# Optimization experiments

Measured on AMD Instinct MI355X. Metric: run time of the kernel, lower is better.

## Reference

```python
import jax, jax.numpy as jnp
import numpy as np

H_D, W_D = 64, 64          # 1024x1024 image / 16 patch size
N = H_D * W_D              # 4096 patches
D = 768                    # DINO ViT-B/16 embed dim
ALPHA = 0.5
K = 100


def setup_inputs() -> dict:
    key = jax.random.key(0)
    k1, k2 = jax.random.split(key)
    out = jax.random.normal(k1, (N, D), dtype=jnp.float32)
    attn_seed = jax.random.randint(k2, (2,), 0, H_D, dtype=jnp.int32)
    return {"out": out, "attn_seed": attn_seed}


def _connected_components(mask):
    """8-connectivity connected components via iterative min-label propagation.
    Background = 0. Foreground pixels get the minimum initial id (+1) of their
    component (same partition as cv2.connectedComponents, different numbering)."""
    fg = mask > 0
    BIG = jnp.int32(N + 1)
    init = jnp.where(fg, jnp.arange(N, dtype=jnp.int32).reshape(H_D, W_D) + 1, BIG)

    def step(l):
        p = jnp.pad(l, 1, constant_values=N + 1)
        m = l
        for dy in (0, 1, 2):          # fixed 3x3 neighborhood, not a data-dim loop
            for dx in (0, 1, 2):
                m = jnp.minimum(m, p[dy:dy + H_D, dx:dx + W_D])
        return jnp.where(fg, m, BIG)

    def cond(st):
        l, prev = st
        return jnp.any(l != prev)

    def body(st):
        l, _ = st
        return step(l), l

    l, _ = jax.lax.while_loop(cond, body, (step(init), init))
    return jnp.where(fg, l, 0)


def reference(out, attn_seed):
    # similarity between all patch features: [N, N]
    sim = out @ out.T
    deg = sim >= 0                                        # degree_matrix (bool)
    # patch with fewest non-negative similarities
    seed_degree_flat = jnp.argmin(deg.sum(axis=0)).astype(jnp.int32)
    seed_degree = jnp.stack([seed_degree_flat // W_D, seed_degree_flat % W_D])
    # blend degree seed with attention seed
    seed_rc = jnp.round(ALPHA * seed_degree + (1.0 - ALPHA) * attn_seed).astype(jnp.int32)
    seed = seed_rc[0] * W_D + seed_rc[1]

    # initial expansion set = patches positively correlated with the seed
    s = deg[seed].astype(jnp.int32)
    s = s.at[seed].set(1)                                 # degree_matrix[seed][seed] = 255 (truthy)
    order = jnp.argsort(-sim[seed])                       # descending
    s = s.at[order[K:]].set(0)                            # keep top-k most similar

    # sequential seed expansion (updates feed into later iterations)
    def step(s, i):
        grows = jnp.sum(sim[i] * (s == 1)) > 0
        s = s.at[i].set(jnp.where(s[i] == 0, 0, jnp.where(grows, 1, 0)))
        return s, None

    s, _ = jax.lax.scan(step, s, jnp.arange(N))

    return _connected_components(s.reshape(H_D, W_D))
```

## Files before the change

kernel.cpp:

```cpp
#include <hip/hip_runtime.h>
#include <cstdint>

#define NP   4096
#define DD   768
#define HD   64
#define WD   64
#define KTOP 100
#define BIGL 4097

typedef short bf16x8 __attribute__((ext_vector_type(8)));
typedef float f32x4  __attribute__((ext_vector_type(4)));

__device__ __forceinline__ void gload_lds16(const void* g, void* l) {
    __builtin_amdgcn_global_load_lds(
        (const __attribute__((address_space(1))) unsigned int*)(uintptr_t)g,
        (__attribute__((address_space(3))) unsigned int*)(unsigned int)(uintptr_t)l,
        16, 0, 0);
}

__device__ __forceinline__ unsigned short f2bf_rne(float x) {
    unsigned b = __float_as_uint(x);
    unsigned r = b + 0x7FFFu + ((b >> 16) & 1u);
    return (unsigned short)(r >> 16);
}
__device__ __forceinline__ float bf2f(unsigned short h) {
    return __uint_as_float(((unsigned)h) << 16);
}

__global__ __launch_bounds__(256) void k_split(const float* __restrict__ A,
                                               unsigned short* __restrict__ hi,
                                               unsigned short* __restrict__ lo,
                                               int* __restrict__ counts) {
    if (blockIdx.x < 16) counts[blockIdx.x * 256 + threadIdx.x] = 0;
    int idx = blockIdx.x * 256 + threadIdx.x;
    float4 v = ((const float4*)A)[idx];
    unsigned short h0 = f2bf_rne(v.x), h1 = f2bf_rne(v.y),
                   h2 = f2bf_rne(v.z), h3 = f2bf_rne(v.w);
    unsigned short l0 = f2bf_rne(v.x - bf2f(h0)), l1 = f2bf_rne(v.y - bf2f(h1)),
                   l2 = f2bf_rne(v.z - bf2f(h2)), l3 = f2bf_rne(v.w - bf2f(h3));
    ((ushort4*)hi)[idx] = make_ushort4(h0, h1, h2, h3);
    ((ushort4*)lo)[idx] = make_ushort4(l0, l1, l2, l3);
}

__device__ __forceinline__ void stage_group(const unsigned short* __restrict__ hi,
                                            const unsigned short* __restrict__ lo,
                                            int i0, int j0, int kbase, int tid,
                                            unsigned short* G) {
#pragma unroll
    for (int q = 0; q < 8; ++q) {
        int pp = q * 256 + tid;
        int ppt = pp & 1023;
        int row = ppt >> 3;
        int kcl = (ppt & 7) ^ (row & 7);
        int rbase = (pp < 1024) ? i0 : j0;
        const unsigned short* src =
            ((kcl < 4) ? hi : lo) + (size_t)(rbase + row) * DD + kbase + (kcl & 3) * 8;
        gload_lds16(src, G + pp * 8);
    }
}

__global__ __launch_bounds__(256, 2) void k_gemm(const unsigned short* __restrict__ hi,
                                                 const unsigned short* __restrict__ lo,
                                                 int* __restrict__ counts) {
    __shared__ __align__(16) unsigned short G[2][2048 * 8];

    int t = ((blockIdx.x & 7) * 66) + (blockIdx.x >> 3);
    int SI = 0, SJ = 0, rem = t;
    for (;;) {
        int sz = (SI == SJ) ? 36 : 64;
        if (rem < sz) break;
        rem -= sz;
        if (++SJ == 4) { ++SI; SJ = SI; }
    }
    int li, lj;
    if (SI == SJ) {
        int r = 0;
        while (rem >= (8 - r)) { rem -= (8 - r); ++r; }
        li = r; lj = r + rem;
    } else { li = rem >> 3; lj = rem & 7; }
    int bi = SI * 8 + li, bj = SJ * 8 + lj;
    int i0 = bi * 128, j0 = bj * 128;

    int tid = threadIdx.x;
    int lane = tid & 63, w = tid >> 6;
    int wm = w & 1, wn = w >> 1;

    f32x4 acc[4][4];
#pragma unroll
    for (int ti = 0; ti < 4; ++ti)
#pragma unroll
        for (int u = 0; u < 4; ++u) { acc[ti][u][0] = 0.f; acc[ti][u][1] = 0.f;
                                      acc[ti][u][2] = 0.f; acc[ti][u][3] = 0.f; }

    int kcf = lane >> 4;
    int paH[4], paL[4], pbH[4], pbL[4];
#pragma unroll
    for (int tt = 0; tt < 4; ++tt) {
        int arow = wm * 64 + tt * 16 + (lane & 15);
        paH[tt] = arow * 8 + (kcf ^ (arow & 7));
        paL[tt] = arow * 8 + ((kcf + 4) ^ (arow & 7));
    }
#pragma unroll
    for (int u = 0; u < 4; ++u) {
        int brow = wn * 64 + u * 16 + (lane & 15);
        pbH[u] = 1024 + brow * 8 + (kcf ^ (brow & 7));
        pbL[u] = 1024 + brow * 8 + ((kcf + 4) ^ (brow & 7));
    }

    stage_group(hi, lo, i0, j0, 0, tid, G[0]);
    for (int it = 0; it < 24; ++it) {
        int cur = it & 1;
        asm volatile("s_waitcnt vmcnt(0)" ::: "memory");
        __builtin_amdgcn_s_barrier();

        bf16x8 ahi[4], alo[4], bhi[4], blo[4];
#pragma unroll
        for (int tt = 0; tt < 4; ++tt) {
            ahi[tt] = *(const bf16x8*)&G[cur][paH[tt] * 8];
            alo[tt] = *(const bf16x8*)&G[cur][paL[tt] * 8];
        }
#pragma unroll
        for (int u = 0; u < 4; ++u) {
            bhi[u] = *(const bf16x8*)&G[cur][pbH[u] * 8];
            blo[u] = *(const bf16x8*)&G[cur][pbL[u] * 8];
        }

        if (it + 1 < 24)
            stage_group(hi, lo, i0, j0, (it + 1) * 32, tid, G[cur ^ 1]);

        __builtin_amdgcn_s_setprio(1);
#pragma unroll
        for (int ti = 0; ti < 4; ++ti)
#pragma unroll
            for (int u = 0; u < 4; ++u) {
                acc[ti][u] = __builtin_amdgcn_mfma_f32_16x16x32_bf16(
                    ahi[ti], bhi[u], acc[ti][u], 0, 0, 0);
                acc[ti][u] = __builtin_amdgcn_mfma_f32_16x16x32_bf16(
                    alo[ti], bhi[u], acc[ti][u], 0, 0, 0);
                acc[ti][u] = __builtin_amdgcn_mfma_f32_16x16x32_bf16(
                    ahi[ti], blo[u], acc[ti][u], 0, 0, 0);
            }
        __builtin_amdgcn_s_setprio(0);
    }

    __syncthreads();
    int* colc = (int*)&G[0][0];
    int* rowc = ((int*)&G[0][0]) + 128;
    if (tid < 128) { colc[tid] = 0; rowc[tid] = 0; }
    __syncthreads();

    int nl = lane & 15;
    int rg = lane >> 4;
#pragma unroll
    for (int u = 0; u < 4; ++u) {
        int v = 0;
#pragma unroll
        for (int ti = 0; ti < 4; ++ti) {
            f32x4 a = acc[ti][u];
            v += ((a[0] >= 0.f) ? 1 : 0) + ((a[1] >= 0.f) ? 1 : 0) +
                 ((a[2] >= 0.f) ? 1 : 0) + ((a[3] >= 0.f) ? 1 : 0);
        }
        v += __shfl_xor(v, 16);
        v += __shfl_xor(v, 32);
        if (rg == 0) atomicAdd(&colc[wn * 64 + u * 16 + nl], v);
    }
    if (bi != bj) {
#pragma unroll
        for (int ti = 0; ti < 4; ++ti)
#pragma unroll
            for (int g = 0; g < 4; ++g) {
                int rv = ((acc[ti][0][g] >= 0.f) ? 1 : 0) +
                         ((acc[ti][1][g] >= 0.f) ? 1 : 0) +
                         ((acc[ti][2][g] >= 0.f) ? 1 : 0) +
                         ((acc[ti][3][g] >= 0.f) ? 1 : 0);
                rv += __shfl_xor(rv, 1);
                rv += __shfl_xor(rv, 2);
                rv += __shfl_xor(rv, 4);
                rv += __shfl_xor(rv, 8);
                if (nl == 0) atomicAdd(&rowc[wm * 64 + ti * 16 + rg * 4 + g], rv);
            }
    }
    __syncthreads();
    if (tid < 128) {
        atomicAdd(&counts[j0 + tid], colc[tid]);
        if (bi != bj) atomicAdd(&counts[i0 + tid], rowc[tid]);
    }
}

__device__ __forceinline__ int block_sum256(int v, int lane, int w, int* wred) {
#pragma unroll
    for (int o = 1; o < 64; o <<= 1) v += __shfl_xor(v, o);
    if (lane == 0) wred[w] = v;
    __syncthreads();
    int tt = wred[0] + wred[1] + wred[2] + wred[3];
    __syncthreads();
    return tt;
}
__device__ __forceinline__ int block_exscan256(int v, int lane, int w, int* wred,
                                               int* total) {
    int inc = v;
#pragma unroll
    for (int o = 1; o < 64; o <<= 1) { int u = __shfl_up(inc, o); if (lane >= o) inc += u; }
    if (lane == 63) wred[w] = inc;
    __syncthreads();
    int w0 = wred[0], w1 = wred[1], w2 = wred[2], w3 = wred[3];
    int wofs = (w > 0 ? w0 : 0) + (w > 1 ? w1 : 0) + (w > 2 ? w2 : 0);
    *total = w0 + w1 + w2 + w3;
    __syncthreads();
    return wofs + inc - v;
}

__global__ __launch_bounds__(256) void k_seedrow(const float* __restrict__ A,
                                                 const int* __restrict__ counts,
                                                 const int* __restrict__ attn_seed,
                                                 float* __restrict__ simrow,
                                                 int* __restrict__ seedp,
                                                 int* __restrict__ outp) {
    __shared__ int redA[256], redB[256];
    int tid = threadIdx.x, lane = tid & 63, w = tid >> 6;
    int blk = blockIdx.x;

    int bc = 0x7fffffff, bI = 0;
    for (int j = tid; j < NP; j += 256) {
        int c = counts[j];
        if (c < bc) { bc = c; bI = j; }
    }
    redA[tid] = bc; redB[tid] = bI;
    __syncthreads();
    for (int st = 128; st > 0; st >>= 1) {
        if (tid < st) {
            if (redA[tid + st] < redA[tid] ||
                (redA[tid + st] == redA[tid] && redB[tid + st] < redB[tid])) {
                redA[tid] = redA[tid + st];
                redB[tid] = redB[tid + st];
            }
        }
        __syncthreads();
    }
    int flat = redB[0];
    int sr = flat / WD, sc = flat % WD;
    int vr = sr + attn_seed[0];
    int vc = sc + attn_seed[1];
    int rr, rc;
    if ((vr & 1) == 0) rr = vr >> 1;
    else { int m = vr >> 1; rr = (m & 1) ? m + 1 : m; }
    if ((vc & 1) == 0) rc = vc >> 1;
    else { int m = vc >> 1; rc = (m & 1) ? m + 1 : m; }
    int seed = rr * WD + rc;
    if (blk == 0 && tid == 0) seedp[0] = seed;

    float sv[12];
#pragma unroll
    for (int kk = 0; kk < 12; ++kk) sv[kk] = A[(size_t)seed * DD + lane + kk * 64];
    int jbase = blk * 32 + w * 8;
    for (int jj = 0; jj < 8; ++jj) {
        int j = jbase + jj;
        float sum = 0.f;
#pragma unroll
        for (int kk = 0; kk < 12; ++kk)
            sum += sv[kk] * A[(size_t)j * DD + lane + kk * 64];
#pragma unroll
        for (int o = 32; o > 0; o >>= 1) sum += __shfl_down(sum, o);
        if (lane == 0) simrow[j] = sum;
    }
    if (tid < 32) outp[blk * 32 + tid] = 0;
}

__global__ __launch_bounds__(256) void k_subsel(const float* __restrict__ A,
                                                const float* __restrict__ simrow,
                                                const int* __restrict__ seedp,
                                                int* __restrict__ act, int* __restrict__ Mp,
                                                float* __restrict__ subsim) {
    __shared__ int wred[4];
    __shared__ int act_s[128];
    __shared__ float av[DD];
    int tid = threadIdx.x, lane = tid & 63, w = tid >> 6;
    int seed = seedp[0];
    int base = tid * 16;
    unsigned key[16];
#pragma unroll
    for (int n = 0; n < 16; ++n) {
        unsigned b = __float_as_uint(simrow[base + n]);
        key[n] = (b & 0x80000000u) ? ~b : (b | 0x80000000u);
    }
    unsigned prefix = 0;
    for (int bit = 31; bit >= 0; --bit) {
        unsigned cand = prefix | (1u << bit);
        int c = 0;
#pragma unroll
        for (int n = 0; n < 16; ++n) c += (key[n] >= cand) ? 1 : 0;
        int tot = block_sum256(c, lane, w, wred);
        if (tot >= KTOP) prefix = cand;
    }
    unsigned KT = prefix;
    int cgt = 0, ceq = 0;
#pragma unroll
    for (int n = 0; n < 16; ++n) {
        cgt += (key[n] > KT) ? 1 : 0;
        ceq += (key[n] == KT) ? 1 : 0;
    }
    int totgt = block_sum256(cgt, lane, w, wred);
    int slots = KTOP - totgt;
    int dummy;
    int eqrun = block_exscan256(ceq, lane, w, wred, &dummy);
    int flag[16]; int cf = 0;
#pragma unroll
    for (int n = 0; n < 16; ++n) {
        int j = base + n;
        unsigned k = key[n];
        int topk = (k > KT) || (k == KT && eqrun < slots);
        if (k == KT) ++eqrun;
        int f = (topk && (k >= 0x80000000u || j == seed)) ? 1 : 0;
        flag[n] = f; cf += f;
    }
    int M;
    int off = block_exscan256(cf, lane, w, wred, &M);
#pragma unroll
    for (int n = 0; n < 16; ++n)
        if (flag[n]) act_s[off++] = base + n;
    __syncthreads();

    int p = blockIdx.x;
    if (p == 0) {
        if (tid == 0) Mp[0] = M;
        if (tid < M) act[tid] = act_s[tid];
    }
    if (p >= M) return;

    int ip = act_s[p];
    for (int k = tid; k < DD; k += 256) av[k] = A[(size_t)ip * DD + k];
    __syncthreads();
    for (int q = w; q < M; q += 4) {
        int iq = act_s[q];
        float sum = 0.f;
#pragma unroll
        for (int kk = 0; kk < 12; ++kk) {
            int k = lane + kk * 64;
            sum += av[k] * A[(size_t)iq * DD + k];
        }
#pragma unroll
        for (int o = 32; o > 0; o >>= 1) sum += __shfl_down(sum, o);
        if (lane == 0) subsim[p * 128 + q] = sum;
    }
}

__global__ __launch_bounds__(256) void k_fin(const float* __restrict__ subsim,
                                             const int* __restrict__ act,
                                             const int* __restrict__ Mp,
                                             int* __restrict__ outp) {
    __shared__ float ss[128 * 128];
    __shared__ int act_s[128];
    __shared__ int alive[128];
    __shared__ int lab[128];
    __shared__ unsigned char nbr[128][8];
    __shared__ int ncnt[128];
    __shared__ int chg;
    int M = Mp[0];
    int tid = threadIdx.x, lane = tid & 63;

    if (tid < 128) act_s[tid] = (tid < M) ? act[tid] : 0;
    for (int i4 = tid; i4 < M * 32; i4 += 256) {
        int p = i4 >> 5, qb = (i4 & 31) << 2;
        float4 v = ((const float4*)subsim)[i4];
        ss[(qb + 0) * 128 + ((p + qb + 0) & 127)] = v.x;
        ss[(qb + 1) * 128 + ((p + qb + 1) & 127)] = v.y;
        ss[(qb + 2) * 128 + ((p + qb + 2) & 127)] = v.z;
        ss[(qb + 3) * 128 + ((p + qb + 3) & 127)] = v.w;
    }
    __syncthreads();

    if (tid < 64) {
        float S_lo = 0.f, S_hi = 0.f;
        for (int q = 0; q < M; ++q) {
            S_lo += ss[q * 128 + ((lane + q) & 127)];
            S_hi += ss[q * 128 + ((lane + 64 + q) & 127)];
        }
        float al = (lane < M) ? 1.f : 0.f;
        float ah = (lane + 64 < M) ? 1.f : 0.f;
        for (int p = 0; p < M; ++p) {
            float Sp = (p < 64) ? __shfl(S_lo, p) : __shfl(S_hi, p - 64);
            if (!(Sp > 0.f)) {
                S_lo -= ss[p * 128 + ((lane + p) & 127)];
                S_hi -= ss[p * 128 + ((lane + 64 + p) & 127)];
                if (lane == p)      al = 0.f;
                if (lane + 64 == p) ah = 0.f;
            }
        }
        alive[lane]      = (lane < M && al != 0.f) ? 1 : 0;
        alive[lane + 64] = (lane + 64 < M && ah != 0.f) ? 1 : 0;
    }
    __syncthreads();

    if (tid < 128) {
        int a = (tid < M) ? alive[tid] : 0;
        int c = 0;
        if (a) {
            int id = act_s[tid];
            int y = id >> 6, x = id & 63;
            for (int q = 0; q < M; ++q) {
                if (q == tid || !alive[q]) continue;
                int qid = act_s[q];
                int dy = (qid >> 6) - y, dx = (qid & 63) - x;
                if (dy >= -1 && dy <= 1 && dx >= -1 && dx <= 1)
                    nbr[tid][c++] = (unsigned char)q;
            }
        }
        ncnt[tid] = c;
        lab[tid] = a ? tid : 32767;
    }
    __syncthreads();
    while (true) {
        if (tid == 0) chg = 0;
        __syncthreads();
        int local = 0;
        if (tid < M && alive[tid]) {
            int m = lab[tid];
            int nc = ncnt[tid];
            for (int k = 0; k < nc; ++k) { int u = lab[nbr[tid][k]]; if (u < m) m = u; }
            { int u = lab[m]; if (u < m) m = u; }
            { int u = lab[m]; if (u < m) m = u; }
            if (m < lab[tid]) { lab[tid] = m; local = 1; }
        }
        if (local) chg = 1;
        __syncthreads();
        if (chg == 0) break;
        __syncthreads();
    }
    if (tid < M && alive[tid]) outp[act_s[tid]] = act_s[lab[tid]] + 1;
}

extern "C" void kernel_launch(void* const* d_in, const int* in_sizes, int n_in,
                              void* d_out, int out_size, void* d_ws, size_t ws_size,
                              hipStream_t stream) {
    const float* A = (const float*)d_in[0];
    const int* attn = (const int*)d_in[1];
    int* outp = (int*)d_out;

    char* ws = (char*)d_ws;
    int*            counts = (int*)(ws);
    float*          simrow = (float*)(ws + 16384);
    int*            act    = (int*)(ws + 32768);
    int*            Mp     = (int*)(ws + 33280);
    int*            seedp  = (int*)(ws + 33284);
    float*          subsim = (float*)(ws + 33792);
    unsigned short* hi     = (unsigned short*)(ws + 1048576);
    unsigned short* lo     = (unsigned short*)(ws + 1048576 + 6291456);

    k_split  <<<3072, 256, 0, stream>>>(A, hi, lo, counts);
    k_gemm   <<<528,  256, 0, stream>>>(hi, lo, counts);
    k_seedrow<<<128,  256, 0, stream>>>(A, counts, attn, simrow, seedp, outp);
    k_subsel <<<128,  256, 0, stream>>>(A, simrow, seedp, act, Mp, subsim);
    k_fin    <<<1,    256, 0, stream>>>(subsim, act, Mp, outp);
}
```

Before: 191.0 us.

## Fuse bf16 split into GEMM loads and merge tail kernels cooperatively

The separate split kernel that wrote hi/lo bf16 copies of the input is removed. The GEMM now loads fp32 tiles into registers, converts them to hi/lo bf16 and writes them to LDS itself, overlapping the next tile's global loads with the MFMA loop. The three tail kernels (seed row, subset selection, finalisation) become one cooperative kernel with grid-wide syncs, and counts is zeroed with a memset. This cuts the intermediate hi/lo traffic and launch overhead, but adds per-iteration conversion ALU work, gives up the direct global-to-LDS async loads, and adds cooperative-launch grid syncs.

```diff
diff --git a/kernel.cpp b/kernel.cpp
--- a/kernel.cpp
+++ b/kernel.cpp
@@ -1,22 +1,17 @@
 #include <hip/hip_runtime.h>
+#include <hip/hip_cooperative_groups.h>
 #include <cstdint>
+
+namespace cg = cooperative_groups;
 
 #define NP   4096
 #define DD   768
 #define HD   64
 #define WD   64
 #define KTOP 100
-#define BIGL 4097
 
 typedef short bf16x8 __attribute__((ext_vector_type(8)));
 typedef float f32x4  __attribute__((ext_vector_type(4)));
-
-__device__ __forceinline__ void gload_lds16(const void* g, void* l) {
-    __builtin_amdgcn_global_load_lds(
-        (const __attribute__((address_space(1))) unsigned int*)(uintptr_t)g,
-        (__attribute__((address_space(3))) unsigned int*)(unsigned int)(uintptr_t)l,
-        16, 0, 0);
-}
 
 __device__ __forceinline__ unsigned short f2bf_rne(float x) {
     unsigned b = __float_as_uint(x);
@@ -27,40 +22,7 @@
     return __uint_as_float(((unsigned)h) << 16);
 }
 
-__global__ __launch_bounds__(256) void k_split(const float* __restrict__ A,
-                                               unsigned short* __restrict__ hi,
-                                               unsigned short* __restrict__ lo,
-                                               int* __restrict__ counts) {
-    if (blockIdx.x < 16) counts[blockIdx.x * 256 + threadIdx.x] = 0;
-    int idx = blockIdx.x * 256 + threadIdx.x;
-    float4 v = ((const float4*)A)[idx];
-    unsigned short h0 = f2bf_rne(v.x), h1 = f2bf_rne(v.y),
-                   h2 = f2bf_rne(v.z), h3 = f2bf_rne(v.w);
-    unsigned short l0 = f2bf_rne(v.x - bf2f(h0)), l1 = f2bf_rne(v.y - bf2f(h1)),
-                   l2 = f2bf_rne(v.z - bf2f(h2)), l3 = f2bf_rne(v.w - bf2f(h3));
-    ((ushort4*)hi)[idx] = make_ushort4(h0, h1, h2, h3);
-    ((ushort4*)lo)[idx] = make_ushort4(l0, l1, l2, l3);
-}
-
-__device__ __forceinline__ void stage_group(const unsigned short* __restrict__ hi,
-                                            const unsigned short* __restrict__ lo,
-                                            int i0, int j0, int kbase, int tid,
-                                            unsigned short* G) {
-#pragma unroll
-    for (int q = 0; q < 8; ++q) {
-        int pp = q * 256 + tid;
-        int ppt = pp & 1023;
-        int row = ppt >> 3;
-        int kcl = (ppt & 7) ^ (row & 7);
-        int rbase = (pp < 1024) ? i0 : j0;
-        const unsigned short* src =
-            ((kcl < 4) ? hi : lo) + (size_t)(rbase + row) * DD + kbase + (kcl & 3) * 8;
-        gload_lds16(src, G + pp * 8);
-    }
-}
-
-__global__ __launch_bounds__(256, 2) void k_gemm(const unsigned short* __restrict__ hi,
-                                                 const unsigned short* __restrict__ lo,
+__global__ __launch_bounds__(256, 2) void k_gemm(const float* __restrict__ A,
                                                  int* __restrict__ counts) {
     __shared__ __align__(16) unsigned short G[2][2048 * 8];
 
@@ -107,10 +69,45 @@
         pbL[u] = 1024 + brow * 8 + ((kcf + 4) ^ (brow & 7));
     }
 
-    stage_group(hi, lo, i0, j0, 0, tid, G[0]);
+    const float* srcp[4];
+    int wofH[4], wofL[4];
+#pragma unroll
+    for (int q = 0; q < 4; ++q) {
+        int pq = q * 256 + tid;
+        int panel = pq >> 9;
+        int rowc = pq & 511;
+        int row = rowc >> 2, c = rowc & 3;
+        srcp[q] = A + (size_t)((panel ? j0 : i0) + row) * DD + c * 8;
+        int base = panel * 1024 + row * 8, sw = row & 7;
+        wofH[q] = (base + (c ^ sw)) * 8;
+        wofL[q] = (base + ((c + 4) ^ sw)) * 8;
+    }
+
+    float4 rg[4][2];
+#pragma unroll
+    for (int q = 0; q < 4; ++q) {
+        rg[q][0] = ((const float4*)srcp[q])[0];
+        rg[q][1] = ((const float4*)srcp[q])[1];
+    }
+    asm volatile("s_waitcnt vmcnt(0)" ::: "memory");
+#pragma unroll
+    for (int q = 0; q < 4; ++q) {
+        float vv[8] = {rg[q][0].x, rg[q][0].y, rg[q][0].z, rg[q][0].w,
+                       rg[q][1].x, rg[q][1].y, rg[q][1].z, rg[q][1].w};
+        bf16x8 hv, lv;
+#pragma unroll
+        for (int e = 0; e < 8; ++e) {
+            unsigned short h = f2bf_rne(vv[e]);
+            hv[e] = (short)h;
+            lv[e] = (short)f2bf_rne(vv[e] - bf2f(h));
+        }
+        *(bf16x8*)&G[0][wofH[q]] = hv;
+        *(bf16x8*)&G[0][wofL[q]] = lv;
+    }
+
     for (int it = 0; it < 24; ++it) {
         int cur = it & 1;
-        asm volatile("s_waitcnt vmcnt(0)" ::: "memory");
+        asm volatile("s_waitcnt lgkmcnt(0)" ::: "memory");
         __builtin_amdgcn_s_barrier();
 
         bf16x8 ahi[4], alo[4], bhi[4], blo[4];
@@ -125,8 +122,14 @@
             blo[u] = *(const bf16x8*)&G[cur][pbL[u] * 8];
         }
 
-        if (it + 1 < 24)
-            stage_group(hi, lo, i0, j0, (it + 1) * 32, tid, G[cur ^ 1]);
+        if (it + 1 < 24) {
+            int kb = (it + 1) * 32;
+#pragma unroll
+            for (int q = 0; q < 4; ++q) {
+                rg[q][0] = ((const float4*)(srcp[q] + kb))[0];
+                rg[q][1] = ((const float4*)(srcp[q] + kb))[1];
+            }
+        }
 
         __builtin_amdgcn_s_setprio(1);
 #pragma unroll
@@ -141,6 +144,24 @@
                     ahi[ti], blo[u], acc[ti][u], 0, 0, 0);
             }
         __builtin_amdgcn_s_setprio(0);
+
+        if (it + 1 < 24) {
+            asm volatile("s_waitcnt vmcnt(0)" ::: "memory");
+#pragma unroll
+            for (int q = 0; q < 4; ++q) {
+                float vv[8] = {rg[q][0].x, rg[q][0].y, rg[q][0].z, rg[q][0].w,
+                               rg[q][1].x, rg[q][1].y, rg[q][1].z, rg[q][1].w};
+                bf16x8 hv, lv;
+#pragma unroll
+                for (int e = 0; e < 8; ++e) {
+                    unsigned short h = f2bf_rne(vv[e]);
+                    hv[e] = (short)h;
+                    lv[e] = (short)f2bf_rne(vv[e] - bf2f(h));
+                }
+                *(bf16x8*)&G[cur ^ 1][wofH[q]] = hv;
+                *(bf16x8*)&G[cur ^ 1][wofL[q]] = lv;
+            }
+        }
     }
 
     __syncthreads();
@@ -150,7 +171,7 @@
     __syncthreads();
 
     int nl = lane & 15;
-    int rg = lane >> 4;
+    int rg2 = lane >> 4;
 #pragma unroll
     for (int u = 0; u < 4; ++u) {
         int v = 0;
@@ -162,7 +183,7 @@
         }
         v += __shfl_xor(v, 16);
         v += __shfl_xor(v, 32);
-        if (rg == 0) atomicAdd(&colc[wn * 64 + u * 16 + nl], v);
+        if (rg2 == 0) atomicAdd(&colc[wn * 64 + u * 16 + nl], v);
     }
     if (bi != bj) {
 #pragma unroll
@@ -177,7 +198,7 @@
                 rv += __shfl_xor(rv, 2);
                 rv += __shfl_xor(rv, 4);
                 rv += __shfl_xor(rv, 8);
-                if (nl == 0) atomicAdd(&rowc[wm * 64 + ti * 16 + rg * 4 + g], rv);
+                if (nl == 0) atomicAdd(&rowc[wm * 64 + ti * 16 + rg2 * 4 + g], rv);
             }
     }
     __syncthreads();
@@ -210,13 +231,21 @@
     return wofs + inc - v;
 }
 
-__global__ __launch_bounds__(256) void k_seedrow(const float* __restrict__ A,
-                                                 const int* __restrict__ counts,
-                                                 const int* __restrict__ attn_seed,
-                                                 float* __restrict__ simrow,
-                                                 int* __restrict__ seedp,
-                                                 int* __restrict__ outp) {
+__global__ __launch_bounds__(256) void k_tail(const float* __restrict__ A,
+                                              const int* __restrict__ counts,
+                                              const int* __restrict__ attn_seed,
+                                              float* __restrict__ simrow,
+                                              float* __restrict__ subsim,
+                                              int* __restrict__ outp) {
+    __shared__ float ss[128 * 128];
     __shared__ int redA[256], redB[256];
+    __shared__ int wred[4];
+    __shared__ int act_s[128];
+    __shared__ float av[DD];
+    __shared__ int alive[128], lab[128], ncnt[128];
+    __shared__ unsigned char nbr[128][8];
+    __shared__ int chg;
+
     int tid = threadIdx.x, lane = tid & 63, w = tid >> 6;
     int blk = blockIdx.x;
 
@@ -247,35 +276,27 @@
     if ((vc & 1) == 0) rc = vc >> 1;
     else { int m = vc >> 1; rc = (m & 1) ? m + 1 : m; }
     int seed = rr * WD + rc;
-    if (blk == 0 && tid == 0) seedp[0] = seed;
-
-    float sv[12];
-#pragma unroll
-    for (int kk = 0; kk < 12; ++kk) sv[kk] = A[(size_t)seed * DD + lane + kk * 64];
-    int jbase = blk * 32 + w * 8;
-    for (int jj = 0; jj < 8; ++jj) {
-        int j = jbase + jj;
-        float sum = 0.f;
-#pragma unroll
-        for (int kk = 0; kk < 12; ++kk)
-            sum += sv[kk] * A[(size_t)j * DD + lane + kk * 64];
-#pragma unroll
-        for (int o = 32; o > 0; o >>= 1) sum += __shfl_down(sum, o);
-        if (lane == 0) simrow[j] = sum;
+
+    {
+        float sv[12];
+#pragma unroll
+        for (int kk = 0; kk < 12; ++kk) sv[kk] = A[(size_t)seed * DD + lane + kk * 64];
+        int jbase = blk * 32 + w * 8;
+        for (int jj = 0; jj < 8; ++jj) {
+            int j = jbase + jj;
+            float sum = 0.f;
+#pragma unroll
+            for (int kk = 0; kk < 12; ++kk)
+                sum += sv[kk] * A[(size_t)j * DD + lane + kk * 64];
+#pragma unroll
+            for (int o = 32; o > 0; o >>= 1) sum += __shfl_down(sum, o);
+            if (lane == 0) simrow[j] = sum;
+        }
     }
     if (tid < 32) outp[blk * 32 + tid] = 0;
-}
-
-__global__ __launch_bounds__(256) void k_subsel(const float* __restrict__ A,
-                                                const float* __restrict__ simrow,
-                                                const int* __restrict__ seedp,
-                                                int* __restrict__ act, int* __restrict__ Mp,
-                                                float* __restrict__ subsim) {
-    __shared__ int wred[4];
-    __shared__ int act_s[128];
-    __shared__ float av[DD];
-    int tid = threadIdx.x, lane = tid & 63, w = tid >> 6;
-    int seed = seedp[0];
+
+    cg::this_grid().sync();
+
     int base = tid * 16;
     unsigned key[16];
 #pragma unroll
@@ -315,118 +336,104 @@
     }
     int M;
     int off = block_exscan256(cf, lane, w, wred, &M);
+    if (tid < 128) act_s[tid] = 0;
+    __syncthreads();
 #pragma unroll
     for (int n = 0; n < 16; ++n)
         if (flag[n]) act_s[off++] = base + n;
     __syncthreads();
 
-    int p = blockIdx.x;
-    if (p == 0) {
-        if (tid == 0) Mp[0] = M;
-        if (tid < M) act[tid] = act_s[tid];
-    }
-    if (p >= M) return;
-
-    int ip = act_s[p];
-    for (int k = tid; k < DD; k += 256) av[k] = A[(size_t)ip * DD + k];
-    __syncthreads();
-    for (int q = w; q < M; q += 4) {
-        int iq = act_s[q];
-        float sum = 0.f;
-#pragma unroll
-        for (int kk = 0; kk < 12; ++kk) {
-            int k = lane + kk * 64;
-            sum += av[k] * A[(size_t)iq * DD + k];
-        }
-#pragma unroll
-        for (int o = 32; o > 0; o >>= 1) sum += __shfl_down(sum, o);
-        if (lane == 0) subsim[p * 128 + q] = sum;
-    }
-}
-
-__global__ __launch_bounds__(256) void k_fin(const float* __restrict__ subsim,
-                                             const int* __restrict__ act,
-                                             const int* __restrict__ Mp,
-                                             int* __restrict__ outp) {
-    __shared__ float ss[128 * 128];
-    __shared__ int act_s[128];
-    __shared__ int alive[128];
-    __shared__ int lab[128];
-    __shared__ unsigned char nbr[128][8];
-    __shared__ int ncnt[128];
-    __shared__ int chg;
-    int M = Mp[0];
-    int tid = threadIdx.x, lane = tid & 63;
-
-    if (tid < 128) act_s[tid] = (tid < M) ? act[tid] : 0;
-    for (int i4 = tid; i4 < M * 32; i4 += 256) {
-        int p = i4 >> 5, qb = (i4 & 31) << 2;
-        float4 v = ((const float4*)subsim)[i4];
-        ss[(qb + 0) * 128 + ((p + qb + 0) & 127)] = v.x;
-        ss[(qb + 1) * 128 + ((p + qb + 1) & 127)] = v.y;
-        ss[(qb + 2) * 128 + ((p + qb + 2) & 127)] = v.z;
-        ss[(qb + 3) * 128 + ((p + qb + 3) & 127)] = v.w;
-    }
-    __syncthreads();
-
-    if (tid < 64) {
-        float S_lo = 0.f, S_hi = 0.f;
-        for (int q = 0; q < M; ++q) {
-            S_lo += ss[q * 128 + ((lane + q) & 127)];
-            S_hi += ss[q * 128 + ((lane + 64 + q) & 127)];
-        }
-        float al = (lane < M) ? 1.f : 0.f;
-        float ah = (lane + 64 < M) ? 1.f : 0.f;
-        for (int p = 0; p < M; ++p) {
-            float Sp = (p < 64) ? __shfl(S_lo, p) : __shfl(S_hi, p - 64);
-            if (!(Sp > 0.f)) {
-                S_lo -= ss[p * 128 + ((lane + p) & 127)];
-                S_hi -= ss[p * 128 + ((lane + 64 + p) & 127)];
-                if (lane == p)      al = 0.f;
-                if (lane + 64 == p) ah = 0.f;
-            }
-        }
-        alive[lane]      = (lane < M && al != 0.f) ? 1 : 0;
-        alive[lane + 64] = (lane + 64 < M && ah != 0.f) ? 1 : 0;
-    }
-    __syncthreads();
-
-    if (tid < 128) {
-        int a = (tid < M) ? alive[tid] : 0;
-        int c = 0;
-        if (a) {
-            int id = act_s[tid];
-            int y = id >> 6, x = id & 63;
+    int p = blk;
+    if (p < M) {
+        int ip = act_s[p];
+        for (int k = tid; k < DD; k += 256) av[k] = A[(size_t)ip * DD + k];
+        __syncthreads();
+        for (int q = w; q < M; q += 4) {
+            int iq = act_s[q];
+            float sum = 0.f;
+#pragma unroll
+            for (int kk = 0; kk < 12; ++kk) {
+                int k = lane + kk * 64;
+                sum += av[k] * A[(size_t)iq * DD + k];
+            }
+#pragma unroll
+            for (int o = 32; o > 0; o >>= 1) sum += __shfl_down(sum, o);
+            if (lane == 0) subsim[p * 128 + q] = sum;
+        }
+    }
+
+    cg::this_grid().sync();
+
+    if (blk == 0) {
+        for (int i4 = tid; i4 < M * 32; i4 += 256) {
+            int pp = i4 >> 5, qb = (i4 & 31) << 2;
+            float4 v = ((const float4*)subsim)[i4];
+            ss[(qb + 0) * 128 + ((pp + qb + 0) & 127)] = v.x;
+            ss[(qb + 1) * 128 + ((pp + qb + 1) & 127)] = v.y;
+            ss[(qb + 2) * 128 + ((pp + qb + 2) & 127)] = v.z;
+            ss[(qb + 3) * 128 + ((pp + qb + 3) & 127)] = v.w;
+        }
+        __syncthreads();
+
+        if (tid < 64) {
+            float S_lo = 0.f, S_hi = 0.f;
             for (int q = 0; q < M; ++q) {
-                if (q == tid || !alive[q]) continue;
-                int qid = act_s[q];
-                int dy = (qid >> 6) - y, dx = (qid & 63) - x;
-                if (dy >= -1 && dy <= 1 && dx >= -1 && dx <= 1)
-                    nbr[tid][c++] = (unsigned char)q;
-            }
-        }
-        ncnt[tid] = c;
-        lab[tid] = a ? tid : 32767;
-    }
-    __syncthreads();
-    while (true) {
-        if (tid == 0) chg = 0;
+                S_lo += ss[q * 128 + ((lane + q) & 127)];
+                S_hi += ss[q * 128 + ((lane + 64 + q) & 127)];
+            }
+            float al = (lane < M) ? 1.f : 0.f;
+            float ah = (lane + 64 < M) ? 1.f : 0.f;
+            for (int pp = 0; pp < M; ++pp) {
+                float Sp = (pp < 64) ? __shfl(S_lo, pp) : __shfl(S_hi, pp - 64);
+                if (!(Sp > 0.f)) {
+                    S_lo -= ss[pp * 128 + ((lane + pp) & 127)];
+                    S_hi -= ss[pp * 128 + ((lane + 64 + pp) & 127)];
+                    if (lane == pp)      al = 0.f;
+                    if (lane + 64 == pp) ah = 0.f;
+                }
+            }
+            alive[lane]      = (lane < M && al != 0.f) ? 1 : 0;
+            alive[lane + 64] = (lane + 64 < M && ah != 0.f) ? 1 : 0;
+        }
         __syncthreads();
-        int local = 0;
-        if (tid < M && alive[tid]) {
-            int m = lab[tid];
-            int nc = ncnt[tid];
-            for (int k = 0; k < nc; ++k) { int u = lab[nbr[tid][k]]; if (u < m) m = u; }
-            { int u = lab[m]; if (u < m) m = u; }
-            { int u = lab[m]; if (u < m) m = u; }
-            if (m < lab[tid]) { lab[tid] = m; local = 1; }
-        }
-        if (local) chg = 1;
+
+        if (tid < 128) {
+            int a = (tid < M) ? alive[tid] : 0;
+            int c = 0;
+            if (a) {
+                int id = act_s[tid];
+                int y = id >> 6, x = id & 63;
+                for (int q = 0; q < M; ++q) {
+                    if (q == tid || !alive[q]) continue;
+                    int qid = act_s[q];
+                    int dy = (qid >> 6) - y, dx = (qid & 63) - x;
+                    if (dy >= -1 && dy <= 1 && dx >= -1 && dx <= 1)
+                        nbr[tid][c++] = (unsigned char)q;
+                }
+            }
+            ncnt[tid] = c;
+            lab[tid] = a ? tid : 32767;
+        }
         __syncthreads();
-        if (chg == 0) break;
-        __syncthreads();
-    }
-    if (tid < M && alive[tid]) outp[act_s[tid]] = act_s[lab[tid]] + 1;
+        while (true) {
+            if (tid == 0) chg = 0;
+            __syncthreads();
+            int local = 0;
+            if (tid < M && alive[tid]) {
+                int m = lab[tid];
+                int nc = ncnt[tid];
+                for (int k = 0; k < nc; ++k) { int u = lab[nbr[tid][k]]; if (u < m) m = u; }
+                { int u = lab[m]; if (u < m) m = u; }
+                { int u = lab[m]; if (u < m) m = u; }
+                if (m < lab[tid]) { lab[tid] = m; local = 1; }
+            }
+            if (local) chg = 1;
+            __syncthreads();
+            if (chg == 0) break;
+            __syncthreads();
+        }
+        if (tid < M && alive[tid]) outp[act_s[tid]] = act_s[lab[tid]] + 1;
+    }
 }
 
 extern "C" void kernel_launch(void* const* d_in, const int* in_sizes, int n_in,
@@ -437,18 +444,14 @@
     int* outp = (int*)d_out;
 
     char* ws = (char*)d_ws;
-    int*            counts = (int*)(ws);
-    float*          simrow = (float*)(ws + 16384);
-    int*            act    = (int*)(ws + 32768);
-    int*            Mp     = (int*)(ws + 33280);
-    int*            seedp  = (int*)(ws + 33284);
-    float*          subsim = (float*)(ws + 33792);
-    unsigned short* hi     = (unsigned short*)(ws + 1048576);
-    unsigned short* lo     = (unsigned short*)(ws + 1048576 + 6291456);
-
-    k_split  <<<3072, 256, 0, stream>>>(A, hi, lo, counts);
-    k_gemm   <<<528,  256, 0, stream>>>(hi, lo, counts);
-    k_seedrow<<<128,  256, 0, stream>>>(A, counts, attn, simrow, seedp, outp);
-    k_subsel <<<128,  256, 0, stream>>>(A, simrow, seedp, act, Mp, subsim);
-    k_fin    <<<1,    256, 0, stream>>>(subsim, act, Mp, outp);
-}
+    int*   counts = (int*)(ws);
+    float* simrow = (float*)(ws + 16384);
+    float* subsim = (float*)(ws + 32768);
+
+    hipMemsetAsync(counts, 0, NP * sizeof(int), stream);
+    k_gemm<<<528, 256, 0, stream>>>(A, counts);
+
+    void* args[] = {(void*)&A, (void*)&counts, (void*)&attn,
+                    (void*)&simrow, (void*)&subsim, (void*)&outp};
+    hipLaunchCooperativeKernel((void*)k_tail, dim3(128), dim3(256), args, 0, stream);
+}
```

Result: slower. 260.2 us (+36.2%).

## Retile Gram GEMM to single-wave 64x64 blocks and widen seed-row grid

Applied to the files above, without the earlier changes.

The degree-count GEMM goes from 256-thread blocks on 128x128 upper-triangular tiles to single-wave 64-thread blocks on 64x64 tiles, using 2080 blocks instead of 528. This drops workgroup barriers and the LDS count reduction, and issues the next stage's loads before waiting with vmcnt(16) so loads overlap compute. Counts now go straight to global memory with more atomics. The seed-row kernel uses 512 blocks of 2 rows per wave instead of 128 blocks of 8 rows, for more parallelism. Smaller tiles mean more global and LDS traffic per FLOP and more global atomic contention.

```diff
diff --git a/kernel.cpp b/kernel.cpp
--- a/kernel.cpp
+++ b/kernel.cpp
@@ -6,7 +6,6 @@
 #define HD   64
 #define WD   64
 #define KTOP 100
-#define BIGL 4097
 
 typedef short bf16x8 __attribute__((ext_vector_type(8)));
 typedef float f32x4  __attribute__((ext_vector_type(4)));
@@ -42,149 +41,126 @@
     ((ushort4*)lo)[idx] = make_ushort4(l0, l1, l2, l3);
 }
 
-__device__ __forceinline__ void stage_group(const unsigned short* __restrict__ hi,
-                                            const unsigned short* __restrict__ lo,
-                                            int i0, int j0, int kbase, int tid,
-                                            unsigned short* G) {
-#pragma unroll
-    for (int q = 0; q < 8; ++q) {
-        int pp = q * 256 + tid;
-        int ppt = pp & 1023;
-        int row = ppt >> 3;
-        int kcl = (ppt & 7) ^ (row & 7);
-        int rbase = (pp < 1024) ? i0 : j0;
-        const unsigned short* src =
-            ((kcl < 4) ? hi : lo) + (size_t)(rbase + row) * DD + kbase + (kcl & 3) * 8;
-        gload_lds16(src, G + pp * 8);
-    }
-}
-
-__global__ __launch_bounds__(256, 2) void k_gemm(const unsigned short* __restrict__ hi,
-                                                 const unsigned short* __restrict__ lo,
-                                                 int* __restrict__ counts) {
-    __shared__ __align__(16) unsigned short G[2][2048 * 8];
-
-    int t = ((blockIdx.x & 7) * 66) + (blockIdx.x >> 3);
-    int SI = 0, SJ = 0, rem = t;
-    for (;;) {
-        int sz = (SI == SJ) ? 36 : 64;
-        if (rem < sz) break;
-        rem -= sz;
-        if (++SJ == 4) { ++SI; SJ = SI; }
-    }
-    int li, lj;
-    if (SI == SJ) {
-        int r = 0;
-        while (rem >= (8 - r)) { rem -= (8 - r); ++r; }
-        li = r; lj = r + rem;
-    } else { li = rem >> 3; lj = rem & 7; }
-    int bi = SI * 8 + li, bj = SJ * 8 + lj;
-    int i0 = bi * 128, j0 = bj * 128;
-
-    int tid = threadIdx.x;
-    int lane = tid & 63, w = tid >> 6;
-    int wm = w & 1, wn = w >> 1;
+__global__ __launch_bounds__(64) void k_gemm(const unsigned short* __restrict__ hi,
+                                             const unsigned short* __restrict__ lo,
+                                             int* __restrict__ counts) {
+    __shared__ __align__(16) unsigned short G[2][1024 * 8];
+
+    int t = ((blockIdx.x & 7) * 260) + (blockIdx.x >> 3);
+    int ti = 0, rem = t;
+    while (rem >= 64 - ti) { rem -= 64 - ti; ++ti; }
+    int tj = ti + rem;
+    int i0 = ti * 64, j0 = tj * 64;
+
+    int lane = threadIdx.x;
 
     f32x4 acc[4][4];
 #pragma unroll
-    for (int ti = 0; ti < 4; ++ti)
-#pragma unroll
-        for (int u = 0; u < 4; ++u) { acc[ti][u][0] = 0.f; acc[ti][u][1] = 0.f;
-                                      acc[ti][u][2] = 0.f; acc[ti][u][3] = 0.f; }
+    for (int a = 0; a < 4; ++a)
+#pragma unroll
+        for (int u = 0; u < 4; ++u) { acc[a][u][0] = 0.f; acc[a][u][1] = 0.f;
+                                      acc[a][u][2] = 0.f; acc[a][u][3] = 0.f; }
 
     int kcf = lane >> 4;
     int paH[4], paL[4], pbH[4], pbL[4];
 #pragma unroll
     for (int tt = 0; tt < 4; ++tt) {
-        int arow = wm * 64 + tt * 16 + (lane & 15);
+        int arow = tt * 16 + (lane & 15);
         paH[tt] = arow * 8 + (kcf ^ (arow & 7));
         paL[tt] = arow * 8 + ((kcf + 4) ^ (arow & 7));
     }
 #pragma unroll
     for (int u = 0; u < 4; ++u) {
-        int brow = wn * 64 + u * 16 + (lane & 15);
-        pbH[u] = 1024 + brow * 8 + (kcf ^ (brow & 7));
-        pbL[u] = 1024 + brow * 8 + ((kcf + 4) ^ (brow & 7));
-    }
-
-    stage_group(hi, lo, i0, j0, 0, tid, G[0]);
+        int brow = u * 16 + (lane & 15);
+        pbH[u] = 512 + brow * 8 + (kcf ^ (brow & 7));
+        pbL[u] = 512 + brow * 8 + ((kcf + 4) ^ (brow & 7));
+    }
+
+    int kcl = (lane & 7) ^ ((lane >> 3) & 7);
+    const unsigned short* sbase = (kcl < 4) ? hi : lo;
+    int koff = (kcl & 3) * 8;
+    const unsigned short* srcA = sbase + (size_t)(i0 + (lane >> 3)) * DD + koff;
+    const unsigned short* srcB = sbase + (size_t)(j0 + (lane >> 3)) * DD + koff;
+
+#define STAGE(buf, kb)                                                        \
+    {                                                                         \
+        _Pragma("unroll")                                                     \
+        for (int q = 0; q < 8; ++q)                                           \
+            gload_lds16(srcA + q * 8 * DD + (kb), (buf) + (q * 64 + lane) * 8);\
+        _Pragma("unroll")                                                     \
+        for (int q = 0; q < 8; ++q)                                           \
+            gload_lds16(srcB + q * 8 * DD + (kb), (buf) + ((q + 8) * 64 + lane) * 8);\
+    }
+
+    STAGE(G[0], 0);
     for (int it = 0; it < 24; ++it) {
-        int cur = it & 1;
-        asm volatile("s_waitcnt vmcnt(0)" ::: "memory");
-        __builtin_amdgcn_s_barrier();
+        unsigned short* Gc = G[it & 1];
+        if (it + 1 < 24) {
+            STAGE(G[(it + 1) & 1], (it + 1) * 32);
+            asm volatile("s_waitcnt vmcnt(16)" ::: "memory");
+        } else {
+            asm volatile("s_waitcnt vmcnt(0)" ::: "memory");
+        }
 
         bf16x8 ahi[4], alo[4], bhi[4], blo[4];
 #pragma unroll
         for (int tt = 0; tt < 4; ++tt) {
-            ahi[tt] = *(const bf16x8*)&G[cur][paH[tt] * 8];
-            alo[tt] = *(const bf16x8*)&G[cur][paL[tt] * 8];
+            ahi[tt] = *(const bf16x8*)&Gc[paH[tt] * 8];
+            alo[tt] = *(const bf16x8*)&Gc[paL[tt] * 8];
         }
 #pragma unroll
         for (int u = 0; u < 4; ++u) {
-            bhi[u] = *(const bf16x8*)&G[cur][pbH[u] * 8];
-            blo[u] = *(const bf16x8*)&G[cur][pbL[u] * 8];
-        }
-
-        if (it + 1 < 24)
-            stage_group(hi, lo, i0, j0, (it + 1) * 32, tid, G[cur ^ 1]);
+            bhi[u] = *(const bf16x8*)&Gc[pbH[u] * 8];
+            blo[u] = *(const bf16x8*)&Gc[pbL[u] * 8];
+        }
 
         __builtin_amdgcn_s_setprio(1);
 #pragma unroll
-        for (int ti = 0; ti < 4; ++ti)
+        for (int tt = 0; tt < 4; ++tt)
 #pragma unroll
             for (int u = 0; u < 4; ++u) {
-                acc[ti][u] = __builtin_amdgcn_mfma_f32_16x16x32_bf16(
-                    ahi[ti], bhi[u], acc[ti][u], 0, 0, 0);
-                acc[ti][u] = __builtin_amdgcn_mfma_f32_16x16x32_bf16(
-                    alo[ti], bhi[u], acc[ti][u], 0, 0, 0);
-                acc[ti][u] = __builtin_amdgcn_mfma_f32_16x16x32_bf16(
-                    ahi[ti], blo[u], acc[ti][u], 0, 0, 0);
+                acc[tt][u] = __builtin_amdgcn_mfma_f32_16x16x32_bf16(
+                    ahi[tt], bhi[u], acc[tt][u], 0, 0, 0);
+                acc[tt][u] = __builtin_amdgcn_mfma_f32_16x16x32_bf16(
+                    alo[tt], bhi[u], acc[tt][u], 0, 0, 0);
+                acc[tt][u] = __builtin_amdgcn_mfma_f32_16x16x32_bf16(
+                    ahi[tt], blo[u], acc[tt][u], 0, 0, 0);
             }
         __builtin_amdgcn_s_setprio(0);
     }
 
-    __syncthreads();
-    int* colc = (int*)&G[0][0];
-    int* rowc = ((int*)&G[0][0]) + 128;
-    if (tid < 128) { colc[tid] = 0; rowc[tid] = 0; }
-    __syncthreads();
-
     int nl = lane & 15;
     int rg = lane >> 4;
 #pragma unroll
     for (int u = 0; u < 4; ++u) {
         int v = 0;
 #pragma unroll
-        for (int ti = 0; ti < 4; ++ti) {
-            f32x4 a = acc[ti][u];
+        for (int tt = 0; tt < 4; ++tt) {
+            f32x4 a = acc[tt][u];
             v += ((a[0] >= 0.f) ? 1 : 0) + ((a[1] >= 0.f) ? 1 : 0) +
                  ((a[2] >= 0.f) ? 1 : 0) + ((a[3] >= 0.f) ? 1 : 0);
         }
         v += __shfl_xor(v, 16);
         v += __shfl_xor(v, 32);
-        if (rg == 0) atomicAdd(&colc[wn * 64 + u * 16 + nl], v);
-    }
-    if (bi != bj) {
-#pragma unroll
-        for (int ti = 0; ti < 4; ++ti)
+        if (rg == 0) atomicAdd(&counts[j0 + u * 16 + nl], v);
+    }
+    if (ti != tj) {
+#pragma unroll
+        for (int tt = 0; tt < 4; ++tt)
 #pragma unroll
             for (int g = 0; g < 4; ++g) {
-                int rv = ((acc[ti][0][g] >= 0.f) ? 1 : 0) +
-                         ((acc[ti][1][g] >= 0.f) ? 1 : 0) +
-                         ((acc[ti][2][g] >= 0.f) ? 1 : 0) +
-                         ((acc[ti][3][g] >= 0.f) ? 1 : 0);
+                int rv = ((acc[tt][0][g] >= 0.f) ? 1 : 0) +
+                         ((acc[tt][1][g] >= 0.f) ? 1 : 0) +
+                         ((acc[tt][2][g] >= 0.f) ? 1 : 0) +
+                         ((acc[tt][3][g] >= 0.f) ? 1 : 0);
                 rv += __shfl_xor(rv, 1);
                 rv += __shfl_xor(rv, 2);
                 rv += __shfl_xor(rv, 4);
                 rv += __shfl_xor(rv, 8);
-                if (nl == 0) atomicAdd(&rowc[wm * 64 + ti * 16 + rg * 4 + g], rv);
+                if (nl == 0) atomicAdd(&counts[i0 + tt * 16 + rg * 4 + g], rv);
             }
     }
-    __syncthreads();
-    if (tid < 128) {
-        atomicAdd(&counts[j0 + tid], colc[tid]);
-        if (bi != bj) atomicAdd(&counts[i0 + tid], rowc[tid]);
-    }
+#undef STAGE
 }
 
 __device__ __forceinline__ int block_sum256(int v, int lane, int w, int* wred) {
@@ -252,8 +228,9 @@
     float sv[12];
 #pragma unroll
     for (int kk = 0; kk < 12; ++kk) sv[kk] = A[(size_t)seed * DD + lane + kk * 64];
-    int jbase = blk * 32 + w * 8;
-    for (int jj = 0; jj < 8; ++jj) {
+    int jbase = blk * 8 + w * 2;
+#pragma unroll
+    for (int jj = 0; jj < 2; ++jj) {
         int j = jbase + jj;
         float sum = 0.f;
 #pragma unroll
@@ -263,7 +240,7 @@
         for (int o = 32; o > 0; o >>= 1) sum += __shfl_down(sum, o);
         if (lane == 0) simrow[j] = sum;
     }
-    if (tid < 32) outp[blk * 32 + tid] = 0;
+    if (blk < 128 && tid < 32) outp[blk * 32 + tid] = 0;
 }
 
 __global__ __launch_bounds__(256) void k_subsel(const float* __restrict__ A,
@@ -447,8 +424,8 @@
     unsigned short* lo     = (unsigned short*)(ws + 1048576 + 6291456);
 
     k_split  <<<3072, 256, 0, stream>>>(A, hi, lo, counts);
-    k_gemm   <<<528,  256, 0, stream>>>(hi, lo, counts);
-    k_seedrow<<<128,  256, 0, stream>>>(A, counts, attn, simrow, seedp, outp);
+    k_gemm   <<<2080, 64,  0, stream>>>(hi, lo, counts);
+    k_seedrow<<<512,  256, 0, stream>>>(A, counts, attn, simrow, seedp, outp);
     k_subsel <<<128,  256, 0, stream>>>(A, simrow, seedp, act, Mp, subsim);
     k_fin    <<<1,    256, 0, stream>>>(subsim, act, Mp, outp);
 }
```

Result: slower. 211.4 us (+10.7%).
